# Kernel optimization log

Hardware: AMD Instinct MI355X
Metric: run time of the kernel (lower is better)

## Reference

```python
import jax, jax.numpy as jnp
import numpy as np

NCLASS = 19


def setup_inputs() -> dict:
    key = jax.random.key(0)
    k1, k2 = jax.random.split(key)
    logits = jax.random.normal(k1, (4, NCLASS, 512, 1024), dtype=jnp.float32)
    target = jax.random.randint(k2, (4, 512, 1024), 0, NCLASS, dtype=jnp.int32)
    return {"logits": logits, "target": target}


def reference(logits, target):
    # Faithful to the torch module: per predicted class cls,
    #   cls_vectors    = logits values at all (c, pixel) positions whose
    #                    argmax-predicted class == cls, grouped per sample n
    #   cls_prototype  = scalar mean of those values per sample
    #   cls_center_loss = mean_n || cls_vectors_n - prototype_n ||_2
    # and the total loss sums over classes. The Python loop + boolean masked
    # select is replaced by one fused segmented reduction using the identity
    #   sum((x - m)^2) = S2 - S1^2 / K   with m = S1/K.
    N, C, H, W = logits.shape
    probs = jax.nn.softmax(logits, axis=1)
    preds = jnp.argmax(probs, axis=1)              # (N, H, W) int

    x = logits.reshape(N, C, H * W)
    s1 = jnp.sum(x, axis=1).reshape(-1)            # (N*HW,) sum over channels per pixel
    s2 = jnp.sum(x * x, axis=1).reshape(-1)        # (N*HW,)
    ones = jnp.ones_like(s1)

    # segment id = sample index * C + predicted class  -> N*C segments
    seg = (preds.reshape(N, -1) + jnp.arange(N, dtype=preds.dtype)[:, None] * C).reshape(-1)
    data = jnp.stack([s1, s2, ones], axis=-1)      # (N*HW, 3)
    sums = jax.ops.segment_sum(data, seg, num_segments=N * C)  # (N*C, 3)
    sums = sums.reshape(N, C, 3)
    S1, S2, cnt = sums[..., 0], sums[..., 1], sums[..., 2]      # (N, nclass)

    # each matching pixel contributes C values => K = cnt * C elements per (n, cls)
    K = jnp.maximum(cnt, 1.0) * C
    sq_dev = jnp.maximum(S2 - S1 * S1 / K, 0.0)    # sum of squared deviations
    norms = jnp.where(cnt > 0, jnp.sqrt(sq_dev), 0.0)           # (N, nclass)

    center_loss = jnp.sum(jnp.mean(norms, axis=0))  # sum over classes of mean over N
    return center_loss
```

## Files before the change

kernel.cpp:

```cpp
#include <hip/hip_runtime.h>

#define NCLS 19
#define NSMP 4
#define HW   (512 * 1024)
#define NSEG (NSMP * NCLS)

__global__ __launch_bounds__(512, 8) void cl_main(const float* __restrict__ logits,
                                                  float* __restrict__ ws) {
    __shared__ float sb[3 * NCLS];
    const int tid = threadIdx.x;
    if (tid < 3 * NCLS) sb[tid] = 0.0f;
    __syncthreads();

    const int    n   = blockIdx.x >> 9;
    const size_t off = ((size_t)(blockIdx.x & 511)) * 1024 + (size_t)tid * 2;
    const float* base = logits + (size_t)n * NCLS * HW + off;

    float2 v[NCLS];
    #pragma unroll
    for (int c = 0; c < NCLS; ++c) {
        v[c] = *(const float2*)(base + (size_t)c * HW);
    }
    asm volatile("" ::: "memory");

    float s1[2], s2[2], mv[2];
    int   mi[2];
    {
        const float a0[2] = {v[0].x, v[0].y};
        #pragma unroll
        for (int j = 0; j < 2; ++j) {
            s1[j] = a0[j];
            s2[j] = a0[j] * a0[j];
            mv[j] = a0[j];
            mi[j] = 0;
        }
    }
    #pragma unroll
    for (int c = 1; c < NCLS; ++c) {
        const float a[2] = {v[c].x, v[c].y};
        #pragma unroll
        for (int j = 0; j < 2; ++j) {
            s1[j] += a[j];
            s2[j]  = fmaf(a[j], a[j], s2[j]);
            if (a[j] > mv[j]) { mv[j] = a[j]; mi[j] = c; }
        }
    }

    #pragma unroll
    for (int j = 0; j < 2; ++j) {
        atomicAdd(&sb[mi[j]],      s1[j]);
        atomicAdd(&sb[19 + mi[j]], s2[j]);
        atomicAdd(&sb[38 + mi[j]], 1.0f);
    }
    __syncthreads();

    if (tid < NCLS) {
        const int seg = n * NCLS + tid;
        atomicAdd(&ws[seg],            sb[tid]);
        atomicAdd(&ws[NSEG + seg],     sb[19 + tid]);
        atomicAdd(&ws[2 * NSEG + seg], sb[38 + tid]);
    }
}

__global__ void cl_final(const float* __restrict__ ws, float* __restrict__ out) {
    __shared__ float red[128];
    const int i = threadIdx.x;
    float v = 0.0f;
    if (i < NSEG) {
        const float S1  = ws[i];
        const float S2  = ws[NSEG + i];
        const float cnt = ws[2 * NSEG + i];
        const float K   = fmaxf(cnt, 1.0f) * (float)NCLS;
        const float sq  = fmaxf(S2 - S1 * S1 / K, 0.0f);
        v = (cnt > 0.0f) ? sqrtf(sq) : 0.0f;
    }
    red[i] = v;
    __syncthreads();
    #pragma unroll
    for (int s = 64; s > 0; s >>= 1) {
        if (i < s) red[i] += red[i + s];
        __syncthreads();
    }
    if (i == 0) out[0] = red[0] / (float)NSMP;
}

extern "C" void kernel_launch(void* const* d_in, const int* in_sizes, int n_in,
                              void* d_out, int out_size, void* d_ws, size_t ws_size,
                              hipStream_t stream) {
    const float* logits = (const float*)d_in[0];
    float* ws  = (float*)d_ws;
    float* out = (float*)d_out;

    hipMemsetAsync(ws, 0, 3 * NSEG * sizeof(float), stream);
    cl_main<<<2048, 512, 0, stream>>>(logits, ws);
    cl_final<<<1, 128, 0, stream>>>(ws, out);
}
```

Measured before the change: 57.86 us.

## Stage logits into LDS with direct global-to-LDS loads and smaller blocks

Logits are no longer loaded into per-thread registers. The kernel now issues 16-byte `global_load_lds` transfers that copy each block's 19×512 tile straight into shared memory, and each thread then reduces two pixels from LDS. Blocks shrink to 256 threads covering 512 pixels, with twice as many blocks. The aim is to cut register pressure and rely on wide asynchronous loads to keep memory busy. In exchange, each block uses about 38 KB of LDS, which limits resident blocks per CU and may lower the number of bytes in flight.

```diff
diff --git a/kernel.cpp b/kernel.cpp
--- a/kernel.cpp
+++ b/kernel.cpp
@@ -5,52 +5,52 @@
 #define HW   (512 * 1024)
 #define NSEG (NSMP * NCLS)
 
-__global__ __launch_bounds__(512, 8) void cl_main(const float* __restrict__ logits,
-                                                  float* __restrict__ ws) {
+__global__ __launch_bounds__(256) void cl_main(const float* __restrict__ logits,
+                                               float* __restrict__ ws) {
+    __shared__ float ch[NCLS * 512];
     __shared__ float sb[3 * NCLS];
     const int tid = threadIdx.x;
     if (tid < 3 * NCLS) sb[tid] = 0.0f;
-    __syncthreads();
 
-    const int    n   = blockIdx.x >> 9;
-    const size_t off = ((size_t)(blockIdx.x & 511)) * 1024 + (size_t)tid * 2;
+    const int    n    = blockIdx.x >> 10;
+    const size_t off  = (size_t)(blockIdx.x & 1023) * 512;
     const float* base = logits + (size_t)n * NCLS * HW + off;
 
-    float2 v[NCLS];
-    #pragma unroll
-    for (int c = 0; c < NCLS; ++c) {
-        v[c] = *(const float2*)(base + (size_t)c * HW);
+    const int w = tid >> 6;
+    const int l = tid & 63;
+
+    for (int j = w; j < 2 * NCLS; j += 4) {
+        const int c = j >> 1;
+        const int h = j & 1;
+        const float* g = base + (size_t)c * HW + h * 256 + l * 4;
+        __builtin_amdgcn_global_load_lds(
+            (const __attribute__((address_space(1))) void*)g,
+            (__attribute__((address_space(3))) void*)&ch[j * 256],
+            16, 0, 0);
     }
-    asm volatile("" ::: "memory");
+    __syncthreads();
 
     float s1[2], s2[2], mv[2];
     int   mi[2];
-    {
-        const float a0[2] = {v[0].x, v[0].y};
+    #pragma unroll
+    for (int k = 0; k < 2; ++k) {
+        const int p = tid + (k << 8);
+        const float a0 = ch[p];
+        s1[k] = a0; s2[k] = a0 * a0; mv[k] = a0; mi[k] = 0;
         #pragma unroll
-        for (int j = 0; j < 2; ++j) {
-            s1[j] = a0[j];
-            s2[j] = a0[j] * a0[j];
-            mv[j] = a0[j];
-            mi[j] = 0;
-        }
-    }
-    #pragma unroll
-    for (int c = 1; c < NCLS; ++c) {
-        const float a[2] = {v[c].x, v[c].y};
-        #pragma unroll
-        for (int j = 0; j < 2; ++j) {
-            s1[j] += a[j];
-            s2[j]  = fmaf(a[j], a[j], s2[j]);
-            if (a[j] > mv[j]) { mv[j] = a[j]; mi[j] = c; }
+        for (int c = 1; c < NCLS; ++c) {
+            const float a = ch[c * 512 + p];
+            s1[k] += a;
+            s2[k]  = fmaf(a, a, s2[k]);
+            if (a > mv[k]) { mv[k] = a; mi[k] = c; }
         }
     }
 
     #pragma unroll
-    for (int j = 0; j < 2; ++j) {
-        atomicAdd(&sb[mi[j]],      s1[j]);
-        atomicAdd(&sb[19 + mi[j]], s2[j]);
-        atomicAdd(&sb[38 + mi[j]], 1.0f);
+    for (int k = 0; k < 2; ++k) {
+        atomicAdd(&sb[mi[k]],      s1[k]);
+        atomicAdd(&sb[19 + mi[k]], s2[k]);
+        atomicAdd(&sb[38 + mi[k]], 1.0f);
     }
     __syncthreads();
 
@@ -92,6 +92,6 @@
     float* out = (float*)d_out;
 
     hipMemsetAsync(ws, 0, 3 * NSEG * sizeof(float), stream);
-    cl_main<<<2048, 512, 0, stream>>>(logits, ws);
+    cl_main<<<4096, 256, 0, stream>>>(logits, ws);
     cl_final<<<1, 128, 0, stream>>>(ws, out);
 }
```

Result: slower. 80.59 us (+39.3%).
